# Kernel tuning notes

Hardware: AMD Instinct MI355X
Metric: run time of the kernel (lower is better)

Reference implementation:

```python
import jax, jax.numpy as jnp
import numpy as np

HEADSIZE = 64  # per-head feature size (attention dim)
KSIZE, STRIDE, PAD = 3, 1, 1


def setup_inputs() -> dict:
    key = jax.random.key(0)
    k1, k2, k3 = jax.random.split(key, 3)
    B, C, T, H, W = 2, 128, 16, 28, 28
    heads = C // HEADSIZE  # 2
    x = jax.random.normal(k1, (B, C, T, H, W), jnp.float32)
    # learned aggregator query (TokenAggregator, size=1), xavier-normal-ish scale
    q = jax.random.normal(k2, (heads, 1, HEADSIZE), jnp.float32) * (2.0 / (1 + HEADSIZE)) ** 0.5
    # output channel projection (MultiHeadLinear-style, heads=1)
    W_out = jax.random.normal(k3, (C, C), jnp.float32) * (2.0 / (C + C)) ** 0.5
    b_out = jnp.zeros((C,), jnp.float32)
    return {"x": x, "q": q, "W_out": W_out, "b_out": b_out}


def _unfold3d(x, k, s, p):
    # torch unfold-via-identity-conv3d equivalent: [B,C,T,H,W] -> [B,C,k^3,To,Ho,Wo]
    B, C, T, H, W = x.shape
    xp = jnp.pad(x, ((0, 0), (0, 0), (p, p), (p, p), (p, p)))
    To = (T + 2 * p - k) // s + 1
    Ho = (H + 2 * p - k) // s + 1
    Wo = (W + 2 * p - k) // s + 1
    taps = []
    for i in range(k):
        for j in range(k):
            for l in range(k):
                taps.append(xp[:, :, i:i + To * s:s, j:j + Ho * s:s, l:l + Wo * s:s])
    return jnp.stack(taps, axis=2)  # [B, C, K, To, Ho, Wo], K = k^3


def reference(x, q, W_out, b_out):
    patches = _unfold3d(x, KSIZE, STRIDE, PAD)          # [B, C, K, To, Ho, Wo]
    B, C, K, To, Ho, Wo = patches.shape
    hs = HEADSIZE
    heads = C // hs
    # tokenize: per spatial location, K window taps are tokens with C channels
    t = patches.transpose(0, 3, 4, 5, 2, 1)             # [B, To, Ho, Wo, K, C]
    # split_heads(headsize): channel dim C -> (headsize slow, heads fast)
    th = t.reshape(B, To, Ho, Wo, K, hs, heads)         # [..., K, hs, heads]
    scale = hs ** -0.5
    # qkv_aggregate: scale applied to BOTH q and k (effective 1/d), softmax over taps
    logits = jnp.einsum('hoc,btuvkch->btuvhok', q * scale, th * scale)  # [B,To,Ho,Wo,heads,1,K]
    attn = jax.nn.softmax(logits, axis=-1)
    res = jnp.einsum('btuvhok,btuvkch->btuvhoc', attn, th)              # [B,To,Ho,Wo,heads,1,hs]
    # merge_heads: channel order (hs slow, head fast) matches the split ordering
    merged = res[:, :, :, :, :, 0, :].transpose(0, 1, 2, 3, 5, 4).reshape(B, To, Ho, Wo, hs * heads)
    # output channel projection
    y = merged @ W_out.T + b_out                         # [B, To, Ho, Wo, C]
    return y.transpose(0, 4, 1, 2, 3)                    # [B, C, To, Ho, Wo]
```

## Files before the change

kernel.cpp:

```cpp
#include <hip/hip_runtime.h>


#define TT 16
#define HH 28
#define WW 28
#define CC 128
#define SP (TT * HH * WW)
#define NPOS (2 * SP)
#define HS 64
#define KT 27
#define MTS 136

typedef __attribute__((ext_vector_type(8))) short bf16x8;
typedef __attribute__((ext_vector_type(4))) float f32x4;

__device__ __forceinline__ unsigned short bf16_rtne(float f) {
    unsigned u = __float_as_uint(f);
    unsigned r = (u + 0x7FFFu + ((u >> 16) & 1u)) >> 16;
    return (unsigned short)r;
}

__global__ __launch_bounds__(256) void qfieldw_kernel(
    const float* __restrict__ x, const float* __restrict__ q,
    float* __restrict__ s,
    const float* __restrict__ Wout, unsigned short* __restrict__ Wb)
{
    if (blockIdx.x >= 784) {
        const int i = (blockIdx.x - 784) * 256 + threadIdx.x;
        Wb[i] = bf16_rtne(Wout[i]);
        return;
    }
    __shared__ float sp[16][32];
    const int tid = threadIdx.x;
    const int pl  = tid & 31;
    const int g   = tid >> 5;
    const int p   = blockIdx.x * 32 + pl;
    const int b   = p / SP;
    const int si  = p % SP;
    const float* xb = x + (size_t)b * CC * SP + si;

    float acc0 = 0.f, acc1 = 0.f;
    #pragma unroll
    for (int j = 0; j < 16; ++j) {
        const int c = g * 16 + j;
        const float val = xb[(size_t)c * SP];
        const float qv  = q[(c & 1) * HS + (c >> 1)] * (1.0f / 64.0f);
        if (c & 1) acc1 += qv * val; else acc0 += qv * val;
    }
    sp[g][pl]     = acc0;
    sp[8 + g][pl] = acc1;
    __syncthreads();
    if (tid < 64) {
        const int h = tid >> 5, pp = tid & 31;
        float a = 0.f;
        #pragma unroll
        for (int g2 = 0; g2 < 8; ++g2) a += sp[h * 8 + g2][pp];
        s[h * NPOS + blockIdx.x * 32 + pp] = a;
    }
}

__global__ __launch_bounds__(256) void fusedmp_kernel(
    const float* __restrict__ x, const float* __restrict__ s,
    const unsigned short* __restrict__ Wb, const float* __restrict__ bout,
    float* __restrict__ out)
{
    __shared__ float s_aw[KT][2][32];
    __shared__ unsigned short s_mt[32][MTS];

    const int pb  = (blockIdx.x & 7) * 98 + (blockIdx.x >> 3);
    const int b   = pb / (SP / 32);
    const int p0  = (pb % (SP / 32)) * 32;
    const int tid = threadIdx.x;

    if (tid < 64) {
        const int h  = tid >> 5;
        const int pl = tid & 31;
        const int p  = p0 + pl;
        const int v = p % WW, u = (p / WW) % HH, t = p / (WW * HH);
        const float* sf = s + h * NPOS + b * SP;
        float l[KT], msk[KT];
        #pragma unroll
        for (int k = 0; k < KT; ++k) {
            const int dt = k / 9 - 1, du = (k / 3) % 3 - 1, dv = k % 3 - 1;
            const int tt = t + dt, uu = u + du, vv = v + dv;
            const bool ok = (unsigned)tt < TT && (unsigned)uu < HH && (unsigned)vv < WW;
            l[k]   = ok ? sf[(tt * HH + uu) * WW + vv] : 0.f;
            msk[k] = ok ? 1.f : 0.f;
        }
        float m = l[0];
        #pragma unroll
        for (int k = 1; k < KT; ++k) m = fmaxf(m, l[k]);
        float sum = 0.f;
        #pragma unroll
        for (int k = 0; k < KT; ++k) { l[k] = __expf(l[k] - m); sum += l[k]; }
        const float inv = 1.f / sum;
        #pragma unroll
        for (int k = 0; k < KT; ++k)
            s_aw[k][h][pl] = l[k] * inv * msk[k];
    }
    __syncthreads();

    {
        const int cg  = tid >> 3;
        const int p4g = tid & 7;
        const int p   = p0 + p4g * 4;
        const int v0  = p % WW;
        const int u   = (p / WW) % HH;
        const int t   = p / (WW * HH);
        const int h   = cg & 1;
        const float* xc0 = x + (size_t)(b * CC + cg) * SP;
        const int vl = (v0 == 0)  ? 0  : v0 - 1;
        const int vr = (v0 == 24) ? 27 : v0 + 4;

        float4 acc[4] = { make_float4(0.f,0.f,0.f,0.f), make_float4(0.f,0.f,0.f,0.f),
                          make_float4(0.f,0.f,0.f,0.f), make_float4(0.f,0.f,0.f,0.f) };

        #pragma unroll
        for (int dt = -1; dt <= 1; ++dt) {
            #pragma unroll
            for (int du = -1; du <= 1; ++du) {
                const int tt = t + dt, uu = u + du;
                const bool rok = ((unsigned)tt < TT) && ((unsigned)uu < HH);
                const int rbase = rok ? (tt * HH + uu) * WW : 0;
                const int kb = ((dt + 1) * 3 + (du + 1)) * 3;
                const float4 wm = *(const float4*)&s_aw[kb + 0][h][p4g * 4];
                const float4 w0 = *(const float4*)&s_aw[kb + 1][h][p4g * 4];
                const float4 wp = *(const float4*)&s_aw[kb + 2][h][p4g * 4];
                #pragma unroll
                for (int ci = 0; ci < 4; ++ci) {
                    const float* xc = xc0 + (size_t)(32 * ci) * SP;
                    const float4 a  = *(const float4*)&xc[rbase + v0];
                    const float  xl = xc[rbase + vl];
                    const float  xr = xc[rbase + vr];
                    acc[ci].x += wm.x * xl;  acc[ci].y += wm.y * a.x;
                    acc[ci].z += wm.z * a.y; acc[ci].w += wm.w * a.z;
                    acc[ci].x += w0.x * a.x; acc[ci].y += w0.y * a.y;
                    acc[ci].z += w0.z * a.z; acc[ci].w += w0.w * a.w;
                    acc[ci].x += wp.x * a.y; acc[ci].y += wp.y * a.z;
                    acc[ci].z += wp.z * a.w; acc[ci].w += wp.w * xr;
                }
            }
        }
        #pragma unroll
        for (int ci = 0; ci < 4; ++ci) {
            const int c = cg + 32 * ci;
            s_mt[p4g * 4 + 0][c] = bf16_rtne(acc[ci].x);
            s_mt[p4g * 4 + 1][c] = bf16_rtne(acc[ci].y);
            s_mt[p4g * 4 + 2][c] = bf16_rtne(acc[ci].z);
            s_mt[p4g * 4 + 3][c] = bf16_rtne(acc[ci].w);
        }
    }
    __syncthreads();

    const int w    = tid >> 6;
    const int lane = tid & 63;
    const int lr   = lane & 15;
    const int lk   = lane >> 4;

    #pragma unroll
    for (int ci2 = 0; ci2 < 2; ++ci2) {
        const int cot = w * 2 + ci2;
        const int cob = cot * 16 + lk * 4;
        f32x4 acc0, acc1;
        #pragma unroll
        for (int r = 0; r < 4; ++r) { acc0[r] = bout[cob + r]; acc1[r] = acc0[r]; }

        #pragma unroll
        for (int ks = 0; ks < 4; ++ks) {
            const bf16x8 aA = *(const bf16x8*)&Wb[(size_t)(cot * 16 + lr) * CC + ks * 32 + lk * 8];
            const bf16x8 b0 = *(const bf16x8*)&s_mt[lr     ][ks * 32 + lk * 8];
            const bf16x8 b1 = *(const bf16x8*)&s_mt[16 + lr][ks * 32 + lk * 8];
            acc0 = __builtin_amdgcn_mfma_f32_16x16x32_bf16(aA, b0, acc0, 0, 0, 0);
            acc1 = __builtin_amdgcn_mfma_f32_16x16x32_bf16(aA, b1, acc1, 0, 0, 0);
        }
        const size_t ob = (size_t)b * CC * SP + p0;
        #pragma unroll
        for (int r = 0; r < 4; ++r) {
            out[ob + (size_t)(cob + r) * SP + lr]      = acc0[r];
            out[ob + (size_t)(cob + r) * SP + 16 + lr] = acc1[r];
        }
    }
}

extern "C" void kernel_launch(void* const* d_in, const int* in_sizes, int n_in,
                              void* d_out, int out_size, void* d_ws, size_t ws_size,
                              hipStream_t stream) {
    const float* x    = (const float*)d_in[0];
    const float* q    = (const float*)d_in[1];
    const float* Wout = (const float*)d_in[2];
    const float* bout = (const float*)d_in[3];
    float* out = (float*)d_out;

    float* s = (float*)d_ws;
    unsigned short* Wb = (unsigned short*)(s + 2 * NPOS);

    qfieldw_kernel<<<dim3(784 + 64),      dim3(256), 0, stream>>>(x, q, s, Wout, Wb);
    fusedmp_kernel<<<dim3(2 * (SP / 32)), dim3(256), 0, stream>>>(x, s, Wb, bout, out);
}
```

Measured before the change: 44.53 us.

## Tile fused kernel by two full spatial rows with per-channel row register reuse

Changes the fused aggregation/projection kernel to process 56 positions (two full W rows) per block instead of 32. Each thread owns one channel and one row, loading each neighbor input row once into registers and reusing it across the three horizontal taps, which removes the redundant edge loads. The GEMM stage now runs four MFMA position tiles per weight fragment, padding the unused rows of the last tile with zeros and masking their stores. Each thread now holds more registers (28 accumulators plus a 28-float row), which may lower occupancy, and the grid shrinks to fewer, larger blocks.

```diff
diff --git a/kernel.cpp b/kernel.cpp
--- a/kernel.cpp
+++ b/kernel.cpp
@@ -9,6 +9,7 @@
 #define NPOS (2 * SP)
 #define HS 64
 #define KT 27
+#define TP 56
 #define MTS 136
 
 typedef __attribute__((ext_vector_type(8))) short bf16x8;
@@ -64,19 +65,27 @@
     const unsigned short* __restrict__ Wb, const float* __restrict__ bout,
     float* __restrict__ out)
 {
-    __shared__ float s_aw[KT][2][32];
-    __shared__ unsigned short s_mt[32][MTS];
-
-    const int pb  = (blockIdx.x & 7) * 98 + (blockIdx.x >> 3);
-    const int b   = pb / (SP / 32);
-    const int p0  = (pb % (SP / 32)) * 32;
-    const int tid = threadIdx.x;
-
-    if (tid < 64) {
-        const int h  = tid >> 5;
-        const int pl = tid & 31;
-        const int p  = p0 + pl;
-        const int v = p % WW, u = (p / WW) % HH, t = p / (WW * HH);
+    __shared__ float s_aw[KT][2][TP];
+    __shared__ unsigned short s_mt[64][MTS];
+
+    const int pb   = (blockIdx.x & 7) * 56 + (blockIdx.x >> 3);
+    const int b    = pb / (SP / TP);
+    const int tile = pb % (SP / TP);
+    const int p0   = tile * TP;
+    const int t    = p0 / (HH * WW);
+    const int u0   = (p0 / WW) % HH;
+    const int tid  = threadIdx.x;
+
+    {
+        unsigned* z = (unsigned*)&s_mt[56][0];
+        for (int i = tid; i < 4 * MTS; i += 256) z[i] = 0;
+    }
+
+    if (tid < 2 * TP) {
+        const int h  = tid / TP;
+        const int pl = tid % TP;
+        const int v  = pl % WW;
+        const int u  = u0 + pl / WW;
         const float* sf = s + h * NPOS + b * SP;
         float l[KT], msk[KT];
         #pragma unroll
@@ -101,54 +110,53 @@
     __syncthreads();
 
     {
-        const int cg  = tid >> 3;
-        const int p4g = tid & 7;
-        const int p   = p0 + p4g * 4;
-        const int v0  = p % WW;
-        const int u   = (p / WW) % HH;
-        const int t   = p / (WW * HH);
-        const int h   = cg & 1;
-        const float* xc0 = x + (size_t)(b * CC + cg) * SP;
-        const int vl = (v0 == 0)  ? 0  : v0 - 1;
-        const int vr = (v0 == 24) ? 27 : v0 + 4;
-
-        float4 acc[4] = { make_float4(0.f,0.f,0.f,0.f), make_float4(0.f,0.f,0.f,0.f),
-                          make_float4(0.f,0.f,0.f,0.f), make_float4(0.f,0.f,0.f,0.f) };
+        const int c = tid & 127;
+        const int r = tid >> 7;
+        const int h = c & 1;
+        const float* xc = x + (size_t)(b * CC + c) * SP;
+
+        float acc[28];
+        #pragma unroll
+        for (int p = 0; p < 28; ++p) acc[p] = 0.f;
 
         #pragma unroll
         for (int dt = -1; dt <= 1; ++dt) {
             #pragma unroll
             for (int du = -1; du <= 1; ++du) {
-                const int tt = t + dt, uu = u + du;
+                const int tt = t + dt, uu = u0 + r + du;
                 const bool rok = ((unsigned)tt < TT) && ((unsigned)uu < HH);
                 const int rbase = rok ? (tt * HH + uu) * WW : 0;
+
+                float xrow[28];
+                #pragma unroll
+                for (int j = 0; j < 7; ++j) {
+                    const float4 tmp = *(const float4*)&xc[rbase + 4 * j];
+                    xrow[4 * j + 0] = tmp.x; xrow[4 * j + 1] = tmp.y;
+                    xrow[4 * j + 2] = tmp.z; xrow[4 * j + 3] = tmp.w;
+                }
+
                 const int kb = ((dt + 1) * 3 + (du + 1)) * 3;
-                const float4 wm = *(const float4*)&s_aw[kb + 0][h][p4g * 4];
-                const float4 w0 = *(const float4*)&s_aw[kb + 1][h][p4g * 4];
-                const float4 wp = *(const float4*)&s_aw[kb + 2][h][p4g * 4];
                 #pragma unroll
-                for (int ci = 0; ci < 4; ++ci) {
-                    const float* xc = xc0 + (size_t)(32 * ci) * SP;
-                    const float4 a  = *(const float4*)&xc[rbase + v0];
-                    const float  xl = xc[rbase + vl];
-                    const float  xr = xc[rbase + vr];
-                    acc[ci].x += wm.x * xl;  acc[ci].y += wm.y * a.x;
-                    acc[ci].z += wm.z * a.y; acc[ci].w += wm.w * a.z;
-                    acc[ci].x += w0.x * a.x; acc[ci].y += w0.y * a.y;
-                    acc[ci].z += w0.z * a.z; acc[ci].w += w0.w * a.w;
-                    acc[ci].x += wp.x * a.y; acc[ci].y += wp.y * a.z;
-                    acc[ci].z += wp.z * a.w; acc[ci].w += wp.w * xr;
+                for (int dv = 0; dv < 3; ++dv) {
+                    const int k  = kb + dv;
+                    const int sh = dv - 1;
+                    const float* awr = &s_aw[k][h][r * 28];
+                    #pragma unroll
+                    for (int j = 0; j < 7; ++j) {
+                        const float4 awv = *(const float4*)&awr[4 * j];
+                        const int i0 = 4 * j + 0 + sh, i1 = 4 * j + 1 + sh;
+                        const int i2 = 4 * j + 2 + sh, i3 = 4 * j + 3 + sh;
+                        acc[4 * j + 0] += awv.x * xrow[i0 < 0 ? 0 : i0];
+                        acc[4 * j + 1] += awv.y * xrow[i1];
+                        acc[4 * j + 2] += awv.z * xrow[i2];
+                        acc[4 * j + 3] += awv.w * xrow[i3 > 27 ? 27 : i3];
+                    }
                 }
             }
         }
         #pragma unroll
-        for (int ci = 0; ci < 4; ++ci) {
-            const int c = cg + 32 * ci;
-            s_mt[p4g * 4 + 0][c] = bf16_rtne(acc[ci].x);
-            s_mt[p4g * 4 + 1][c] = bf16_rtne(acc[ci].y);
-            s_mt[p4g * 4 + 2][c] = bf16_rtne(acc[ci].z);
-            s_mt[p4g * 4 + 3][c] = bf16_rtne(acc[ci].w);
-        }
+        for (int p = 0; p < 28; ++p)
+            s_mt[r * 28 + p][c] = bf16_rtne(acc[p]);
     }
     __syncthreads();
 
@@ -161,23 +169,30 @@
     for (int ci2 = 0; ci2 < 2; ++ci2) {
         const int cot = w * 2 + ci2;
         const int cob = cot * 16 + lk * 4;
-        f32x4 acc0, acc1;
-        #pragma unroll
-        for (int r = 0; r < 4; ++r) { acc0[r] = bout[cob + r]; acc1[r] = acc0[r]; }
+        f32x4 acc4[4];
+        #pragma unroll
+        for (int pt = 0; pt < 4; ++pt)
+            #pragma unroll
+            for (int r2 = 0; r2 < 4; ++r2) acc4[pt][r2] = bout[cob + r2];
 
         #pragma unroll
         for (int ks = 0; ks < 4; ++ks) {
             const bf16x8 aA = *(const bf16x8*)&Wb[(size_t)(cot * 16 + lr) * CC + ks * 32 + lk * 8];
-            const bf16x8 b0 = *(const bf16x8*)&s_mt[lr     ][ks * 32 + lk * 8];
-            const bf16x8 b1 = *(const bf16x8*)&s_mt[16 + lr][ks * 32 + lk * 8];
-            acc0 = __builtin_amdgcn_mfma_f32_16x16x32_bf16(aA, b0, acc0, 0, 0, 0);
-            acc1 = __builtin_amdgcn_mfma_f32_16x16x32_bf16(aA, b1, acc1, 0, 0, 0);
+            #pragma unroll
+            for (int pt = 0; pt < 4; ++pt) {
+                const bf16x8 bb = *(const bf16x8*)&s_mt[pt * 16 + lr][ks * 32 + lk * 8];
+                acc4[pt] = __builtin_amdgcn_mfma_f32_16x16x32_bf16(aA, bb, acc4[pt], 0, 0, 0);
+            }
         }
         const size_t ob = (size_t)b * CC * SP + p0;
         #pragma unroll
-        for (int r = 0; r < 4; ++r) {
-            out[ob + (size_t)(cob + r) * SP + lr]      = acc0[r];
-            out[ob + (size_t)(cob + r) * SP + 16 + lr] = acc1[r];
+        for (int pt = 0; pt < 4; ++pt) {
+            const int pos = pt * 16 + lr;
+            if (pt < 3 || lr < 8) {
+                #pragma unroll
+                for (int r2 = 0; r2 < 4; ++r2)
+                    out[ob + (size_t)(cob + r2) * SP + pos] = acc4[pt][r2];
+            }
         }
     }
 }
@@ -195,5 +210,5 @@
     unsigned short* Wb = (unsigned short*)(s + 2 * NPOS);
 
     qfieldw_kernel<<<dim3(784 + 64),      dim3(256), 0, stream>>>(x, q, s, Wout, Wb);
-    fusedmp_kernel<<<dim3(2 * (SP / 32)), dim3(256), 0, stream>>>(x, s, Wb, bout, out);
-}
+    fusedmp_kernel<<<dim3(2 * (SP / TP)), dim3(256), 0, stream>>>(x, s, Wb, bout, out);
+}
```

Result: slower. 121.0 us (+171.8%).

## Retile fused aggregation kernel to one spatial row per block with register sliding window

Applied to the files above, without the earlier changes.

Each block of the fused kernel now covers one full W row (28 positions) instead of 32 linear positions, and each thread handles one channel for half a row. Sixteen values per neighbour row are loaded with float4 reads and reused across the three horizontal taps in registers, which removes the scalar edge loads and row-crossing logic. The last four rows of the MFMA tile are padded with zeros and not stored. The cost is 12.5% more blocks, a partly wasted MFMA tile, and higher register pressure from the 16-wide accumulators and row buffers.

```diff
diff --git a/kernel.cpp b/kernel.cpp
--- a/kernel.cpp
+++ b/kernel.cpp
@@ -14,6 +14,8 @@
 typedef __attribute__((ext_vector_type(8))) short bf16x8;
 typedef __attribute__((ext_vector_type(4))) float f32x4;
 
+#define CLMP(a) ((a) < 0 ? 0 : ((a) > 15 ? 15 : (a)))
+
 __device__ __forceinline__ unsigned short bf16_rtne(float f) {
     unsigned u = __float_as_uint(f);
     unsigned r = (u + 0x7FFFu + ((u >> 16) & 1u)) >> 16;
@@ -59,6 +61,50 @@
     }
 }
 
+template<int HALF>
+__device__ __forceinline__ void phaseB_row(
+    const float* __restrict__ xc, const float (*s_aw)[2][32], int h,
+    int t, int u0, unsigned short (*s_mt)[MTS], int c)
+{
+    float acc[16];
+    #pragma unroll
+    for (int i = 0; i < 16; ++i) acc[i] = 0.f;
+
+    #pragma unroll
+    for (int dt = -1; dt <= 1; ++dt) {
+        #pragma unroll
+        for (int du = -1; du <= 1; ++du) {
+            const int tt = t + dt, uu = u0 + du;
+            const bool rok = ((unsigned)tt < TT) && ((unsigned)uu < HH);
+            const int rbase = rok ? (tt * HH + uu) * WW : 0;
+            float xr[16];
+            #pragma unroll
+            for (int j = 0; j < 4; ++j) {
+                const float4 tmp = *(const float4*)&xc[rbase + HALF * 12 + 4 * j];
+                xr[4*j+0] = tmp.x; xr[4*j+1] = tmp.y;
+                xr[4*j+2] = tmp.z; xr[4*j+3] = tmp.w;
+            }
+            const int kb = ((dt + 1) * 3 + (du + 1)) * 3;
+            #pragma unroll
+            for (int dv = 0; dv < 3; ++dv) {
+                const float4* aw4 = (const float4*)&s_aw[kb + dv][h][HALF * 16];
+                #pragma unroll
+                for (int j = 0; j < 4; ++j) {
+                    const float4 a4 = aw4[j];
+                    const int ib = 4 * j;
+                    acc[ib+0] += a4.x * xr[CLMP(ib+0 + dv - 1 + 2*HALF)];
+                    acc[ib+1] += a4.y * xr[CLMP(ib+1 + dv - 1 + 2*HALF)];
+                    acc[ib+2] += a4.z * xr[CLMP(ib+2 + dv - 1 + 2*HALF)];
+                    acc[ib+3] += a4.w * xr[CLMP(ib+3 + dv - 1 + 2*HALF)];
+                }
+            }
+        }
+    }
+    #pragma unroll
+    for (int i = 0; i < 14; ++i)
+        s_mt[HALF * 14 + i][c] = bf16_rtne(acc[i]);
+}
+
 __global__ __launch_bounds__(256) void fusedmp_kernel(
     const float* __restrict__ x, const float* __restrict__ s,
     const unsigned short* __restrict__ Wb, const float* __restrict__ bout,
@@ -67,22 +113,28 @@
     __shared__ float s_aw[KT][2][32];
     __shared__ unsigned short s_mt[32][MTS];
 
-    const int pb  = (blockIdx.x & 7) * 98 + (blockIdx.x >> 3);
-    const int b   = pb / (SP / 32);
-    const int p0  = (pb % (SP / 32)) * 32;
-    const int tid = threadIdx.x;
-
-    if (tid < 64) {
-        const int h  = tid >> 5;
-        const int pl = tid & 31;
-        const int p  = p0 + pl;
-        const int v = p % WW, u = (p / WW) % HH, t = p / (WW * HH);
+    const int pb   = (blockIdx.x & 7) * 112 + (blockIdx.x >> 3);
+    const int b    = pb / 448;
+    const int tile = pb % 448;
+    const int p0   = tile * 28;
+    const int t    = tile / 28;
+    const int u0   = tile % 28;
+    const int tid  = threadIdx.x;
+
+    {
+        unsigned* z = (unsigned*)&s_mt[28][0];
+        for (int i = tid; i < 2 * MTS; i += 256) z[i] = 0;
+    }
+
+    if (tid < 56) {
+        const int h = tid / 28;
+        const int v = tid % 28;
         const float* sf = s + h * NPOS + b * SP;
         float l[KT], msk[KT];
         #pragma unroll
         for (int k = 0; k < KT; ++k) {
             const int dt = k / 9 - 1, du = (k / 3) % 3 - 1, dv = k % 3 - 1;
-            const int tt = t + dt, uu = u + du, vv = v + dv;
+            const int tt = t + dt, uu = u0 + du, vv = v + dv;
             const bool ok = (unsigned)tt < TT && (unsigned)uu < HH && (unsigned)vv < WW;
             l[k]   = ok ? sf[(tt * HH + uu) * WW + vv] : 0.f;
             msk[k] = ok ? 1.f : 0.f;
@@ -94,61 +146,19 @@
         #pragma unroll
         for (int k = 0; k < KT; ++k) { l[k] = __expf(l[k] - m); sum += l[k]; }
         const float inv = 1.f / sum;
+        const int half = v / 14, vi = v % 14;
         #pragma unroll
         for (int k = 0; k < KT; ++k)
-            s_aw[k][h][pl] = l[k] * inv * msk[k];
+            s_aw[k][h][half * 16 + vi] = l[k] * inv * msk[k];
     }
     __syncthreads();
 
     {
-        const int cg  = tid >> 3;
-        const int p4g = tid & 7;
-        const int p   = p0 + p4g * 4;
-        const int v0  = p % WW;
-        const int u   = (p / WW) % HH;
-        const int t   = p / (WW * HH);
-        const int h   = cg & 1;
-        const float* xc0 = x + (size_t)(b * CC + cg) * SP;
-        const int vl = (v0 == 0)  ? 0  : v0 - 1;
-        const int vr = (v0 == 24) ? 27 : v0 + 4;
-
-        float4 acc[4] = { make_float4(0.f,0.f,0.f,0.f), make_float4(0.f,0.f,0.f,0.f),
-                          make_float4(0.f,0.f,0.f,0.f), make_float4(0.f,0.f,0.f,0.f) };
-
-        #pragma unroll
-        for (int dt = -1; dt <= 1; ++dt) {
-            #pragma unroll
-            for (int du = -1; du <= 1; ++du) {
-                const int tt = t + dt, uu = u + du;
-                const bool rok = ((unsigned)tt < TT) && ((unsigned)uu < HH);
-                const int rbase = rok ? (tt * HH + uu) * WW : 0;
-                const int kb = ((dt + 1) * 3 + (du + 1)) * 3;
-                const float4 wm = *(const float4*)&s_aw[kb + 0][h][p4g * 4];
-                const float4 w0 = *(const float4*)&s_aw[kb + 1][h][p4g * 4];
-                const float4 wp = *(const float4*)&s_aw[kb + 2][h][p4g * 4];
-                #pragma unroll
-                for (int ci = 0; ci < 4; ++ci) {
-                    const float* xc = xc0 + (size_t)(32 * ci) * SP;
-                    const float4 a  = *(const float4*)&xc[rbase + v0];
-                    const float  xl = xc[rbase + vl];
-                    const float  xr = xc[rbase + vr];
-                    acc[ci].x += wm.x * xl;  acc[ci].y += wm.y * a.x;
-                    acc[ci].z += wm.z * a.y; acc[ci].w += wm.w * a.z;
-                    acc[ci].x += w0.x * a.x; acc[ci].y += w0.y * a.y;
-                    acc[ci].z += w0.z * a.z; acc[ci].w += w0.w * a.w;
-                    acc[ci].x += wp.x * a.y; acc[ci].y += wp.y * a.z;
-                    acc[ci].z += wp.z * a.w; acc[ci].w += wp.w * xr;
-                }
-            }
-        }
-        #pragma unroll
-        for (int ci = 0; ci < 4; ++ci) {
-            const int c = cg + 32 * ci;
-            s_mt[p4g * 4 + 0][c] = bf16_rtne(acc[ci].x);
-            s_mt[p4g * 4 + 1][c] = bf16_rtne(acc[ci].y);
-            s_mt[p4g * 4 + 2][c] = bf16_rtne(acc[ci].z);
-            s_mt[p4g * 4 + 3][c] = bf16_rtne(acc[ci].w);
-        }
+        const int c = tid & 127;
+        const int h = c & 1;
+        const float* xc = x + (size_t)(b * CC + c) * SP;
+        if (tid < 128) phaseB_row<0>(xc, s_aw, h, t, u0, s_mt, c);
+        else           phaseB_row<1>(xc, s_aw, h, t, u0, s_mt, c);
     }
     __syncthreads();
 
@@ -175,9 +185,12 @@
         }
         const size_t ob = (size_t)b * CC * SP + p0;
         #pragma unroll
-        for (int r = 0; r < 4; ++r) {
-            out[ob + (size_t)(cob + r) * SP + lr]      = acc0[r];
-            out[ob + (size_t)(cob + r) * SP + 16 + lr] = acc1[r];
+        for (int r = 0; r < 4; ++r)
+            out[ob + (size_t)(cob + r) * SP + lr] = acc0[r];
+        if (lr < 12) {
+            #pragma unroll
+            for (int r = 0; r < 4; ++r)
+                out[ob + (size_t)(cob + r) * SP + 16 + lr] = acc1[r];
         }
     }
 }
@@ -194,6 +207,6 @@
     float* s = (float*)d_ws;
     unsigned short* Wb = (unsigned short*)(s + 2 * NPOS);
 
-    qfieldw_kernel<<<dim3(784 + 64),      dim3(256), 0, stream>>>(x, q, s, Wout, Wb);
-    fusedmp_kernel<<<dim3(2 * (SP / 32)), dim3(256), 0, stream>>>(x, s, Wb, bout, out);
-}
+    qfieldw_kernel<<<dim3(784 + 64), dim3(256), 0, stream>>>(x, q, s, Wout, Wb);
+    fusedmp_kernel<<<dim3(2 * 448),  dim3(256), 0, stream>>>(x, s, Wb, bout, out);
+}
```

Result: no change. 44.06 us (-1.1%).
